# Performance work log

Measured on AMD Instinct MI355X. Metric: run time of the kernel, lower is better.

Reference implementation:

```python
import jax, jax.numpy as jnp
import numpy as np

CHUNK = 4096
DECAY = 0.99
EPS = 1e-5


def setup_inputs() -> dict:
    key = jax.random.key(0)
    k1, k2, k3, k4 = jax.random.split(key, 4)
    z = jax.random.normal(k1, (32, 64, 32, 32), dtype=jnp.float32)
    codebook = jax.random.normal(k2, (8192, 64), dtype=jnp.float32)
    cluster_size = jax.random.uniform(k3, (8192,), dtype=jnp.float32)
    embed_avg = jax.random.normal(k4, (8192, 64), dtype=jnp.float32)
    return {"z": z, "codebook": codebook, "cluster_size": cluster_size, "embed_avg": embed_avg}


def _nearest_indices(vectors, codebook):
    """Chunked fp32 squared-L2 nearest-neighbor search (matches _nearest_indices)."""
    cb = codebook.astype(jnp.float32)
    c2 = jnp.sum(cb * cb, axis=1)  # [K]

    def chunk_fn(chunk):
        v = chunk.astype(jnp.float32)  # [CHUNK, D]
        d = jnp.sum(v * v, axis=1, keepdims=True) + c2[None, :] - 2.0 * (v @ cb.T)
        return jnp.argmin(d, axis=1)

    n, d = vectors.shape  # n divisible by CHUNK by construction
    chunks = vectors.reshape(n // CHUNK, CHUNK, d)
    return jax.lax.map(chunk_fn, chunks).reshape(-1)


def reference(z, codebook, cluster_size, embed_avg):
    B, C, H, W = z.shape
    K = codebook.shape[0]
    # [B,C,H,W] -> [N,C]
    vectors = jnp.transpose(z, (0, 2, 3, 1)).reshape(-1, C)
    N = vectors.shape[0]

    indices = _nearest_indices(vectors, codebook)  # [N] int
    quantized = jnp.transpose(codebook[indices].reshape(B, H, W, C), (0, 3, 1, 2))

    # commitment loss (codebook learned via EMA, so only encoder side differentiable)
    vq_loss = jnp.mean((jax.lax.stop_gradient(quantized) - z) ** 2)
    # straight-through estimator
    quantized_st = z + jax.lax.stop_gradient(quantized - z)

    # code usage statistics
    counts = jax.ops.segment_sum(jnp.ones((N,), jnp.float32), indices, num_segments=K)
    avg_probs = counts / N
    perplexity = jnp.exp(-jnp.sum(avg_probs * jnp.log(avg_probs + 1e-10)))
    active_codes = jnp.sum(counts > 0).astype(jnp.int32)

    # EMA update (scatter-add accumulation + Laplace-smoothed normalization)
    sums = jax.ops.segment_sum(vectors.astype(jnp.float32), indices, num_segments=K)
    new_cluster_size = DECAY * cluster_size + (1.0 - DECAY) * counts
    new_embed_avg = DECAY * embed_avg + (1.0 - DECAY) * sums
    n_total = jnp.sum(new_cluster_size)
    smoothed = (new_cluster_size + EPS) / (n_total + K * EPS) * n_total
    new_codebook = new_embed_avg / smoothed[:, None]

    return (quantized_st, indices, vq_loss, perplexity, active_codes,
            new_codebook, new_cluster_size, new_embed_avg)
```

## Files before the change

kernel.cpp:

```cpp
#include <hip/hip_runtime.h>
#include <math.h>

typedef unsigned short u16;
typedef unsigned int u32;
typedef unsigned long long u64;
typedef __attribute__((ext_vector_type(8))) short short8;
typedef __attribute__((ext_vector_type(4))) float f32x4;

#define NVEC   32768
#define DIMV   64
#define KC     8192
#define NKCH   8
#define CHK    1024
#define HW     1024
#define BPLANE 65536

#define OFF_Q    0
#define OFF_IDX  2097152
#define OFF_LOSS 2129920
#define OFF_PPL  2129921
#define OFF_ACT  2129922
#define OFF_NCB  2129923
#define OFF_NCS  2654211
#define OFF_NEA  2662403

#define WS_COUNTS 0
#define WS_SCAL   8192
#define WS_C2     8200
#define WS_MINP   16400
#define WS_OFFS   81936
#define WS_PERM   90128
#define WS_CBH    122896
#define WS_CBM    385040
#define WS_CBL    647184

__device__ __forceinline__ u16 f2bf(float x) {
    u32 u = __float_as_uint(x);
    u += 0x7fffu + ((u >> 16) & 1u);
    return (u16)(u >> 16);
}
__device__ __forceinline__ float bf2f(u16 h) {
    return __uint_as_float(((u32)h) << 16);
}
__device__ __forceinline__ u32 fmono(float f) {
    u32 b = __float_as_uint(f);
    return (b & 0x80000000u) ? ~b : (b | 0x80000000u);
}

__global__ __launch_bounds__(256) void cbsplit_kernel(const float* __restrict__ cb,
                                                      u16* __restrict__ cbh,
                                                      u16* __restrict__ cbm,
                                                      u16* __restrict__ cbl,
                                                      float* __restrict__ c2) {
    const int t = threadIdx.x;
    const int k = blockIdx.x * 4 + (t >> 6);
    const int d = t & 63;
    const int idx = k * DIMV + d;
    float x = cb[idx];
    u16 hb = f2bf(x);  float fh = bf2f(hb);
    float r1 = x - fh; u16 mb = f2bf(r1); float fm = bf2f(mb);
    float r2 = r1 - fm; u16 lb = f2bf(r2);
    cbh[idx] = hb; cbm[idx] = mb; cbl[idx] = lb;
    float s = x * x;
    for (int off = 32; off > 0; off >>= 1) s += __shfl_down(s, off, 64);
    if (d == 0) c2[k] = s;
}

__global__ __launch_bounds__(256, 2) void nn_kernel(const float* __restrict__ z,
                                                    const u16* __restrict__ cbh,
                                                    const u16* __restrict__ cbm,
                                                    const u16* __restrict__ cbl,
                                                    const float* __restrict__ c2,
                                                    u64* __restrict__ minp) {
    const int l  = threadIdx.x & 63;
    const int w  = threadIdx.x >> 6;
    const int vg = blockIdx.x;
    const int kc = blockIdx.y;
    const int m0 = vg * 256 + w * 64;
    const int lr = l & 15;
    const int lg = l >> 4;

    short8 A[4][3][2];
#pragma unroll
    for (int i = 0; i < 4; ++i) {
        const int vec = m0 + i * 16 + lr;
        const float* zp = z + (size_t)(vec >> 10) * BPLANE + (vec & 1023);
#pragma unroll
        for (int s = 0; s < 2; ++s) {
            short8 ah, am, al;
#pragma unroll
            for (int e = 0; e < 8; ++e) {
                const int k = s * 32 + lg * 8 + e;
                float x = zp[k * HW];
                u16 hb = f2bf(x);   float fh = bf2f(hb);
                float r1 = x - fh;  u16 mb = f2bf(r1); float fm = bf2f(mb);
                float r2 = r1 - fm; u16 lb = f2bf(r2);
                ah[e] = (short)hb; am[e] = (short)mb; al[e] = (short)lb;
            }
            A[i][0][s] = ah; A[i][1][s] = am; A[i][2][s] = al;
        }
    }

    float bestv[4][4];
    int   bestn[4][4];
#pragma unroll
    for (int i = 0; i < 4; ++i)
#pragma unroll
        for (int r = 0; r < 4; ++r) { bestv[i][r] = -3.4e38f; bestn[i][r] = 0; }

    const int code_base = kc * CHK;
    const u16* ph = cbh + (size_t)(code_base + lr) * DIMV + lg * 8;
    const u16* pm = cbm + (size_t)(code_base + lr) * DIMV + lg * 8;
    const u16* pl = cbl + (size_t)(code_base + lr) * DIMV + lg * 8;
    const float* pc2 = c2 + code_base + lr;

    for (int nt = 0; nt < CHK / 16; ++nt) {
        const int to = nt * 16 * DIMV;
        const float cm = -0.5f * pc2[nt * 16];
        short8 Bh0 = *(const short8*)(ph + to);
        short8 Bh1 = *(const short8*)(ph + to + 32);
        short8 Bm0 = *(const short8*)(pm + to);
        short8 Bm1 = *(const short8*)(pm + to + 32);
        short8 Bl0 = *(const short8*)(pl + to);
        short8 Bl1 = *(const short8*)(pl + to + 32);
#pragma unroll
        for (int i = 0; i < 4; ++i) {
            f32x4 acc = {cm, cm, cm, cm};
            acc = __builtin_amdgcn_mfma_f32_16x16x32_bf16(A[i][0][0], Bh0, acc, 0, 0, 0);
            acc = __builtin_amdgcn_mfma_f32_16x16x32_bf16(A[i][0][1], Bh1, acc, 0, 0, 0);
            acc = __builtin_amdgcn_mfma_f32_16x16x32_bf16(A[i][1][0], Bh0, acc, 0, 0, 0);
            acc = __builtin_amdgcn_mfma_f32_16x16x32_bf16(A[i][1][1], Bh1, acc, 0, 0, 0);
            acc = __builtin_amdgcn_mfma_f32_16x16x32_bf16(A[i][0][0], Bm0, acc, 0, 0, 0);
            acc = __builtin_amdgcn_mfma_f32_16x16x32_bf16(A[i][0][1], Bm1, acc, 0, 0, 0);
            acc = __builtin_amdgcn_mfma_f32_16x16x32_bf16(A[i][1][0], Bm0, acc, 0, 0, 0);
            acc = __builtin_amdgcn_mfma_f32_16x16x32_bf16(A[i][1][1], Bm1, acc, 0, 0, 0);
            acc = __builtin_amdgcn_mfma_f32_16x16x32_bf16(A[i][2][0], Bh0, acc, 0, 0, 0);
            acc = __builtin_amdgcn_mfma_f32_16x16x32_bf16(A[i][2][1], Bh1, acc, 0, 0, 0);
            acc = __builtin_amdgcn_mfma_f32_16x16x32_bf16(A[i][0][0], Bl0, acc, 0, 0, 0);
            acc = __builtin_amdgcn_mfma_f32_16x16x32_bf16(A[i][0][1], Bl1, acc, 0, 0, 0);
#pragma unroll
            for (int r = 0; r < 4; ++r) {
                float a = acc[r];
                if (a > bestv[i][r]) { bestv[i][r] = a; bestn[i][r] = nt; }
            }
        }
    }

#pragma unroll
    for (int i = 0; i < 4; ++i)
#pragma unroll
        for (int r = 0; r < 4; ++r) {
            float v = bestv[i][r];
            int idx = bestn[i][r] * 16 + lr;
#pragma unroll
            for (int mk = 1; mk < 16; mk <<= 1) {
                float ov = __shfl_xor(v, mk, 64);
                int   oi = __shfl_xor(idx, mk, 64);
                if (ov > v || (ov == v && oi < idx)) { v = ov; idx = oi; }
            }
            if (lr == 0) {
                const int vec = m0 + i * 16 + lg * 4 + r;
                const u64 pack = ((u64)fmono(-v) << 32) | (u32)(code_base + idx);
                atomicMin(&minp[vec], pack);
            }
        }
}

__global__ __launch_bounds__(256) void gather_kernel(const float* __restrict__ z,
                                                     const float* __restrict__ cb,
                                                     const u64* __restrict__ minp,
                                                     float* __restrict__ out,
                                                     float* __restrict__ counts,
                                                     float* __restrict__ scal) {
    const int n = blockIdx.x * 256 + threadIdx.x;
    const int bi = (int)(u32)(minp[n] & 0xFFFFFFFFu);
    out[OFF_IDX + n] = (float)bi;
    atomicAdd(&counts[bi], 1.0f);

    const int b = n >> 10, h = n & 1023;
    const float* zp = z + (size_t)b * BPLANE + h;
    const float* cp = cb + (size_t)bi * DIMV;
    float* qp = out + OFF_Q + (size_t)b * BPLANE + h;
    float acc = 0.f;
#pragma unroll
    for (int c = 0; c < DIMV; ++c) {
        float zv = zp[c * HW];
        float q = cp[c];
        float df = q - zv;
        acc = fmaf(df, df, acc);
        qp[c * HW] = zv + df;
    }
    for (int off = 32; off > 0; off >>= 1) acc += __shfl_down(acc, off, 64);
    __shared__ float red[4];
    if ((threadIdx.x & 63) == 0) red[threadIdx.x >> 6] = acc;
    __syncthreads();
    if (threadIdx.x == 0) atomicAdd(&scal[0], (red[0] + red[1]) + (red[2] + red[3]));
}

__global__ __launch_bounds__(256) void prefix_kernel(const float* __restrict__ counts,
                                                     int* __restrict__ offs) {
    __shared__ int part[256];
    const int t = threadIdx.x;
    const int base = t * 32;
    int loc[32];
    int s = 0;
#pragma unroll
    for (int j = 0; j < 32; ++j) { loc[j] = s; s += (int)counts[base + j]; }
    part[t] = s;
    __syncthreads();
    for (int off = 1; off < 256; off <<= 1) {
        int v = (t >= off) ? part[t - off] : 0;
        __syncthreads();
        part[t] += v;
        __syncthreads();
    }
    const int excl = part[t] - s;
#pragma unroll
    for (int j = 0; j < 32; ++j) offs[base + j] = excl + loc[j];
}

__global__ __launch_bounds__(256) void scatter_kernel(const float* __restrict__ outIdx,
                                                      int* __restrict__ offs,
                                                      int* __restrict__ perm) {
    const int n = blockIdx.x * 256 + threadIdx.x;
    const int bi = (int)outIdx[n];
    const int pos = atomicAdd(&offs[bi], 1);
    perm[pos] = n;
}

__global__ __launch_bounds__(256) void segsum_kernel(const float* __restrict__ z,
                                                     const float* __restrict__ counts,
                                                     const int* __restrict__ offs,
                                                     const int* __restrict__ perm,
                                                     float* __restrict__ sums) {
    const int w = threadIdx.x >> 6;
    const int c = threadIdx.x & 63;
    const int k = blockIdx.x * 4 + w;
    const int end = offs[k];
    const int cnt = (int)counts[k];
    float s = 0.f;
    for (int m = end - cnt; m < end; ++m) {
        const int n = perm[m];
        s += z[(size_t)(n >> 10) * BPLANE + (size_t)c * HW + (n & 1023)];
    }
    sums[k * DIMV + c] = s;
}

__global__ __launch_bounds__(256) void stats_kernel(const float* __restrict__ cs,
                                                    const float* __restrict__ counts,
                                                    float* __restrict__ out,
                                                    float* __restrict__ scal) {
    const int k = blockIdx.x * 256 + threadIdx.x;
    const float cnt = counts[k];
    float ncs = 0.99f * cs[k] + 0.01f * cnt;
    out[OFF_NCS + k] = ncs;
    float p = cnt * (1.0f / 32768.0f);
    float pl = p * logf(p + 1e-10f);
    float act = (cnt > 0.f) ? 1.f : 0.f;
    for (int off = 32; off > 0; off >>= 1) {
        ncs += __shfl_down(ncs, off, 64);
        pl  += __shfl_down(pl,  off, 64);
        act += __shfl_down(act, off, 64);
    }
    __shared__ float r0[4], r1[4], r2[4];
    const int w = threadIdx.x >> 6;
    if ((threadIdx.x & 63) == 0) { r0[w] = ncs; r1[w] = pl; r2[w] = act; }
    __syncthreads();
    if (threadIdx.x == 0) {
        atomicAdd(&scal[1], (r0[0] + r0[1]) + (r0[2] + r0[3]));
        atomicAdd(&scal[2], (r1[0] + r1[1]) + (r1[2] + r1[3]));
        atomicAdd(&scal[3], (r2[0] + r2[1]) + (r2[2] + r2[3]));
    }
}

__global__ __launch_bounds__(256) void final_kernel(const float* __restrict__ ea,
                                                    const float* __restrict__ sums,
                                                    float* __restrict__ out,
                                                    const float* __restrict__ scal) {
    const int i = blockIdx.x * 256 + threadIdx.x;
    const float nea = 0.99f * ea[i] + 0.01f * sums[i];
    out[OFF_NEA + i] = nea;
    const float nt = scal[1];
    const int k = i >> 6;
    const float ncs = out[OFF_NCS + k];
    const float sm = ((ncs + 1e-5f) / (nt + 0.08192f)) * nt;
    out[OFF_NCB + i] = nea / sm;
    if (i == 0) {
        out[OFF_LOSS] = scal[0] * (1.0f / 2097152.0f);
        out[OFF_PPL]  = expf(-scal[2]);
        out[OFF_ACT]  = scal[3];
    }
}

extern "C" void kernel_launch(void* const* d_in, const int* in_sizes, int n_in,
                              void* d_out, int out_size, void* d_ws, size_t ws_size,
                              hipStream_t stream) {
    const float* z  = (const float*)d_in[0];
    const float* cb = (const float*)d_in[1];
    const float* cs = (const float*)d_in[2];
    const float* ea = (const float*)d_in[3];
    float* out = (float*)d_out;
    float* ws  = (float*)d_ws;

    float* counts = ws + WS_COUNTS;
    float* scal   = ws + WS_SCAL;
    float* c2     = ws + WS_C2;
    u64*   minp   = (u64*)(ws + WS_MINP);
    int*   offs   = (int*)(ws + WS_OFFS);
    int*   perm   = (int*)(ws + WS_PERM);
    u16*   cbh    = (u16*)(ws + WS_CBH);
    u16*   cbm    = (u16*)(ws + WS_CBM);
    u16*   cbl    = (u16*)(ws + WS_CBL);
    float* sums   = ws + WS_CBH;

    hipMemsetAsync(ws, 0, 8200 * 4, stream);
    hipMemsetAsync(minp, 0xFF, NVEC * 8, stream);
    cbsplit_kernel<<<KC / 4, 256, 0, stream>>>(cb, cbh, cbm, cbl, c2);
    nn_kernel<<<dim3(128, NKCH), 256, 0, stream>>>(z, cbh, cbm, cbl, c2, minp);
    gather_kernel<<<NVEC / 256, 256, 0, stream>>>(z, cb, minp, out, counts, scal);
    prefix_kernel<<<1, 256, 0, stream>>>(counts, offs);
    scatter_kernel<<<NVEC / 256, 256, 0, stream>>>(out + OFF_IDX, offs, perm);
    segsum_kernel<<<KC / 4, 256, 0, stream>>>(z, counts, offs, perm, sums);
    stats_kernel<<<KC / 256, 256, 0, stream>>>(cs, counts, out, scal);
    final_kernel<<<524288 / 256, 256, 0, stream>>>(ea, sums, out, scal);
}
```

Before: 303.6 us.

## Double-buffer codebook tile loads and halve code-chunk grid split

The NN search loop now uses two register sets, so the loads for the next 16-code tile are issued before the MFMAs on the current tile run, hiding global load latency. Each block also covers twice as many codes (2048 instead of 1024), which halves the blockIdx.y grid and the number of atomicMin merges per vector. The extra register set raises VGPR pressure under launch_bounds(256,2). The smaller grid may also reduce the parallelism available to hide latency.

```diff
diff --git a/kernel.cpp b/kernel.cpp
--- a/kernel.cpp
+++ b/kernel.cpp
@@ -10,8 +10,8 @@
 #define NVEC   32768
 #define DIMV   64
 #define KC     8192
-#define NKCH   8
-#define CHK    1024
+#define NKCH   4
+#define CHK    2048
 #define HW     1024
 #define BPLANE 65536
 
@@ -66,6 +66,40 @@
     if (d == 0) c2[k] = s;
 }
 
+#define NN_COMPUTE(Bh0, Bh1, Bm0, Bm1, Bl0, Bl1, CM, NTI)                          \
+    _Pragma("unroll")                                                               \
+    for (int i = 0; i < 4; ++i) {                                                   \
+        f32x4 acc = {CM, CM, CM, CM};                                               \
+        acc = __builtin_amdgcn_mfma_f32_16x16x32_bf16(A[i][0][0], Bh0, acc, 0, 0, 0);\
+        acc = __builtin_amdgcn_mfma_f32_16x16x32_bf16(A[i][0][1], Bh1, acc, 0, 0, 0);\
+        acc = __builtin_amdgcn_mfma_f32_16x16x32_bf16(A[i][1][0], Bh0, acc, 0, 0, 0);\
+        acc = __builtin_amdgcn_mfma_f32_16x16x32_bf16(A[i][1][1], Bh1, acc, 0, 0, 0);\
+        acc = __builtin_amdgcn_mfma_f32_16x16x32_bf16(A[i][0][0], Bm0, acc, 0, 0, 0);\
+        acc = __builtin_amdgcn_mfma_f32_16x16x32_bf16(A[i][0][1], Bm1, acc, 0, 0, 0);\
+        acc = __builtin_amdgcn_mfma_f32_16x16x32_bf16(A[i][1][0], Bm0, acc, 0, 0, 0);\
+        acc = __builtin_amdgcn_mfma_f32_16x16x32_bf16(A[i][1][1], Bm1, acc, 0, 0, 0);\
+        acc = __builtin_amdgcn_mfma_f32_16x16x32_bf16(A[i][2][0], Bh0, acc, 0, 0, 0);\
+        acc = __builtin_amdgcn_mfma_f32_16x16x32_bf16(A[i][2][1], Bh1, acc, 0, 0, 0);\
+        acc = __builtin_amdgcn_mfma_f32_16x16x32_bf16(A[i][0][0], Bl0, acc, 0, 0, 0);\
+        acc = __builtin_amdgcn_mfma_f32_16x16x32_bf16(A[i][0][1], Bl1, acc, 0, 0, 0);\
+        _Pragma("unroll")                                                           \
+        for (int r = 0; r < 4; ++r) {                                               \
+            float a = acc[r];                                                       \
+            if (a > bestv[i][r]) { bestv[i][r] = a; bestn[i][r] = (NTI); }          \
+        }                                                                           \
+    }
+
+#define NN_LOAD(Dh0, Dh1, Dm0, Dm1, Dl0, Dl1, DCM, NTI) {                          \
+        const int to_ = (NTI) * 16 * DIMV;                                          \
+        DCM = -0.5f * pc2[(NTI) * 16];                                              \
+        Dh0 = *(const short8*)(ph + to_);                                           \
+        Dh1 = *(const short8*)(ph + to_ + 32);                                      \
+        Dm0 = *(const short8*)(pm + to_);                                           \
+        Dm1 = *(const short8*)(pm + to_ + 32);                                      \
+        Dl0 = *(const short8*)(pl + to_);                                           \
+        Dl1 = *(const short8*)(pl + to_ + 32);                                      \
+    }
+
 __global__ __launch_bounds__(256, 2) void nn_kernel(const float* __restrict__ z,
                                                     const u16* __restrict__ cbh,
                                                     const u16* __restrict__ cbm,
@@ -114,36 +148,21 @@
     const u16* pl = cbl + (size_t)(code_base + lr) * DIMV + lg * 8;
     const float* pc2 = c2 + code_base + lr;
 
-    for (int nt = 0; nt < CHK / 16; ++nt) {
-        const int to = nt * 16 * DIMV;
-        const float cm = -0.5f * pc2[nt * 16];
-        short8 Bh0 = *(const short8*)(ph + to);
-        short8 Bh1 = *(const short8*)(ph + to + 32);
-        short8 Bm0 = *(const short8*)(pm + to);
-        short8 Bm1 = *(const short8*)(pm + to + 32);
-        short8 Bl0 = *(const short8*)(pl + to);
-        short8 Bl1 = *(const short8*)(pl + to + 32);
-#pragma unroll
-        for (int i = 0; i < 4; ++i) {
-            f32x4 acc = {cm, cm, cm, cm};
-            acc = __builtin_amdgcn_mfma_f32_16x16x32_bf16(A[i][0][0], Bh0, acc, 0, 0, 0);
-            acc = __builtin_amdgcn_mfma_f32_16x16x32_bf16(A[i][0][1], Bh1, acc, 0, 0, 0);
-            acc = __builtin_amdgcn_mfma_f32_16x16x32_bf16(A[i][1][0], Bh0, acc, 0, 0, 0);
-            acc = __builtin_amdgcn_mfma_f32_16x16x32_bf16(A[i][1][1], Bh1, acc, 0, 0, 0);
-            acc = __builtin_amdgcn_mfma_f32_16x16x32_bf16(A[i][0][0], Bm0, acc, 0, 0, 0);
-            acc = __builtin_amdgcn_mfma_f32_16x16x32_bf16(A[i][0][1], Bm1, acc, 0, 0, 0);
-            acc = __builtin_amdgcn_mfma_f32_16x16x32_bf16(A[i][1][0], Bm0, acc, 0, 0, 0);
-            acc = __builtin_amdgcn_mfma_f32_16x16x32_bf16(A[i][1][1], Bm1, acc, 0, 0, 0);
-            acc = __builtin_amdgcn_mfma_f32_16x16x32_bf16(A[i][2][0], Bh0, acc, 0, 0, 0);
-            acc = __builtin_amdgcn_mfma_f32_16x16x32_bf16(A[i][2][1], Bh1, acc, 0, 0, 0);
-            acc = __builtin_amdgcn_mfma_f32_16x16x32_bf16(A[i][0][0], Bl0, acc, 0, 0, 0);
-            acc = __builtin_amdgcn_mfma_f32_16x16x32_bf16(A[i][0][1], Bl1, acc, 0, 0, 0);
-#pragma unroll
-            for (int r = 0; r < 4; ++r) {
-                float a = acc[r];
-                if (a > bestv[i][r]) { bestv[i][r] = a; bestn[i][r] = nt; }
-            }
+    const int NT = CHK / 16;
+
+    short8 P_h0, P_h1, P_m0, P_m1, P_l0, P_l1;
+    short8 Q_h0, Q_h1, Q_m0, Q_m1, Q_l0, Q_l1;
+    float cm0, cm1;
+
+    NN_LOAD(P_h0, P_h1, P_m0, P_m1, P_l0, P_l1, cm0, 0)
+
+    for (int nt = 0; nt < NT; nt += 2) {
+        NN_LOAD(Q_h0, Q_h1, Q_m0, Q_m1, Q_l0, Q_l1, cm1, nt + 1)
+        NN_COMPUTE(P_h0, P_h1, P_m0, P_m1, P_l0, P_l1, cm0, nt)
+        if (nt + 2 < NT) {
+            NN_LOAD(P_h0, P_h1, P_m0, P_m1, P_l0, P_l1, cm0, nt + 2)
         }
+        NN_COMPUTE(Q_h0, Q_h1, Q_m0, Q_m1, Q_l0, Q_l1, cm1, nt + 1)
     }
 
 #pragma unroll
```

Result: faster. 295.6 us (-2.6%).
